# Optimization experiments

Measured on AMD Instinct MI355X. Metric: run time of the kernel, lower is better.

The kernel has to match this reference:

```python
import jax, jax.numpy as jnp
import numpy as np

N_NODES = 50000
N_EDGES = 800000
D_IN = 256
D_HID = 256
D_OUT = 256
BN_EPS = 1e-5
NORM_EPS = 1e-12


def _glorot(key, out_dim, in_dim):
    a = np.sqrt(6.0 / (in_dim + out_dim)).astype(np.float32)
    return jax.random.uniform(key, (out_dim, in_dim), jnp.float32, -a, a)


def setup_inputs() -> dict:
    key = jax.random.key(0)
    ks = jax.random.split(key, 8)
    x = jax.random.normal(ks[0], (N_NODES, D_IN), jnp.float32)
    edge_index = jax.random.randint(ks[1], (2, N_EDGES), 0, N_NODES, dtype=jnp.int32)
    batch = jnp.zeros((N_NODES,), jnp.int32)
    return {
        "x": x,
        "W1_l": _glorot(ks[2], D_HID, D_IN),
        "b1_l": jnp.zeros((D_HID,), jnp.float32),
        "W1_r": _glorot(ks[3], D_HID, D_IN),
        "W2_l": _glorot(ks[4], D_OUT, D_HID),
        "b2_l": jnp.zeros((D_OUT,), jnp.float32),
        "W2_r": _glorot(ks[5], D_OUT, D_HID),
        "gamma1": jnp.ones((D_HID,), jnp.float32),
        "beta1": jnp.zeros((D_HID,), jnp.float32),
        "edge_index": edge_index,
        "batch": batch,
    }


def _sage_conv(x, W_l, b_l, W_r, src, dst, n_nodes):
    # PyG SAGEConv (aggr='mean'): out = lin_l(mean_j x_j) + lin_r(x)
    msgs = x[src]                                            # [E, d] gather
    s = jax.ops.segment_sum(msgs, dst, num_segments=n_nodes)  # [N, d] scatter-add
    cnt = jax.ops.segment_sum(jnp.ones((src.shape[0], 1), x.dtype), dst,
                              num_segments=n_nodes)
    agg = jnp.where(cnt > 0, s / jnp.maximum(cnt, 1.0), 0.0)
    return agg @ W_l.T + b_l + x @ W_r.T


def _batch_norm(h, gamma, beta):
    mu = jnp.mean(h, axis=0)
    var = jnp.mean((h - mu) ** 2, axis=0)  # biased, as torch train-mode BN
    return (h - mu) * jax.lax.rsqrt(var + BN_EPS) * gamma + beta


def _l2_normalize(h):
    n = jnp.linalg.norm(h, axis=-1, keepdims=True)
    return h / jnp.maximum(n, NORM_EPS)


def reference(x, W1_l, b1_l, W1_r, W2_l, b2_l, W2_r, gamma1, beta1,
              edge_index, batch):
    n = x.shape[0]
    src, dst = edge_index[0], edge_index[1]
    # layer 1: SAGEConv -> BN (train stats) -> ReLU (dropout = identity in eval)
    h = _sage_conv(x, W1_l, b1_l, W1_r, src, dst, n)
    h = jax.nn.relu(_batch_norm(h, gamma1, beta1))
    # layer 2: SAGEConv -> L2 normalize
    h = _sage_conv(h, W2_l, b2_l, W2_r, src, dst, n)
    node_emb = _l2_normalize(h)
    # global mean pool over batch ids (single graph here), then normalize
    gsum = jax.ops.segment_sum(node_emb, batch, num_segments=1)
    gcnt = jax.ops.segment_sum(jnp.ones((n, 1), node_emb.dtype), batch,
                               num_segments=1)
    graph_emb = _l2_normalize(gsum / jnp.maximum(gcnt, 1.0))
    return node_emb, graph_emb
```

## Files before the change

kernel.cpp:

```cpp
#include <hip/hip_runtime.h>
#include <math.h>

#define NN 50000
#define NE 800000
#define D  256
#define SCB 196

typedef unsigned short u16;
typedef __attribute__((ext_vector_type(8))) short short8;
typedef __attribute__((ext_vector_type(8))) unsigned short u16x8;
typedef __attribute__((ext_vector_type(4))) float f32x4;

__device__ __forceinline__ u16 f2b(float f) {
    unsigned u = __float_as_uint(f);
    return (u16)((u + 0x7FFFu + ((u >> 16) & 1u)) >> 16);
}
__device__ __forceinline__ float b2f(u16 b) {
    return __uint_as_float(((unsigned)b) << 16);
}

__device__ __forceinline__ void gl16(const u16* g, u16* l) {
    __builtin_amdgcn_global_load_lds(
        (const __attribute__((address_space(1))) void*)g,
        (__attribute__((address_space(3))) void*)l, 16, 0, 0);
}

__global__ void degree_kernel(const int* __restrict__ dst, int* __restrict__ deg) {
    int e0 = (blockIdx.x * blockDim.x + threadIdx.x) * 4;
    if (e0 + 3 < NE) {
        int4 d = *(const int4*)&dst[e0];
        atomicAdd(&deg[d.x], 1);
        atomicAdd(&deg[d.y], 1);
        atomicAdd(&deg[d.z], 1);
        atomicAdd(&deg[d.w], 1);
    } else {
        for (int e = e0; e < NE; e++) atomicAdd(&deg[dst[e]], 1);
    }
}

__global__ void scanA_kernel(const int* __restrict__ deg, int* __restrict__ partial) {
    int t = threadIdx.x;
    int i = blockIdx.x * 256 + t;
    int v = (i < NN) ? deg[i] : 0;
#pragma unroll
    for (int o = 32; o; o >>= 1) v += __shfl_xor(v, o);
    __shared__ int sm[4];
    if ((t & 63) == 0) sm[t >> 6] = v;
    __syncthreads();
    if (t == 0) partial[blockIdx.x] = sm[0] + sm[1] + sm[2] + sm[3];
}

__global__ void scanB_kernel(const int* __restrict__ partial, int* __restrict__ base,
                             int* __restrict__ offs) {
    __shared__ int sm[256];
    int t = threadIdx.x;
    int v = (t < SCB) ? partial[t] : 0;
    sm[t] = v;
    __syncthreads();
    for (int off = 1; off < 256; off <<= 1) {
        int u = 0;
        if (t >= off) u = sm[t - off];
        __syncthreads();
        sm[t] += u;
        __syncthreads();
    }
    if (t < SCB) base[t] = sm[t] - v;
    if (t == 255) offs[NN] = sm[255];
}

__global__ void scanC_kernel(const int* __restrict__ deg, const int* __restrict__ base,
                             int* __restrict__ offs, int* __restrict__ cur) {
    __shared__ int sm[256];
    int t = threadIdx.x;
    int i = blockIdx.x * 256 + t;
    int v = (i < NN) ? deg[i] : 0;
    sm[t] = v;
    __syncthreads();
    for (int off = 1; off < 256; off <<= 1) {
        int u = 0;
        if (t >= off) u = sm[t - off];
        __syncthreads();
        sm[t] += u;
        __syncthreads();
    }
    int o = base[blockIdx.x] + sm[t] - v;
    if (i < NN) {
        offs[i] = o;
        cur[i] = o;
    }
}

__global__ void fill_kernel(const int* __restrict__ src, const int* __restrict__ dst,
                            int* __restrict__ cur, int* __restrict__ csr) {
    int e0 = (blockIdx.x * blockDim.x + threadIdx.x) * 4;
    if (e0 + 3 < NE) {
        int4 d = *(const int4*)&dst[e0];
        int4 s = *(const int4*)&src[e0];
        int p0 = atomicAdd(&cur[d.x], 1);
        int p1 = atomicAdd(&cur[d.y], 1);
        int p2 = atomicAdd(&cur[d.z], 1);
        int p3 = atomicAdd(&cur[d.w], 1);
        csr[p0] = s.x;
        csr[p1] = s.y;
        csr[p2] = s.z;
        csr[p3] = s.w;
    } else {
        for (int e = e0; e < NE; e++) {
            int pos = atomicAdd(&cur[dst[e]], 1);
            csr[pos] = src[e];
        }
    }
}

__global__ void wconv_kernel(const float* __restrict__ W1l, const float* __restrict__ W1r,
                             const float* __restrict__ W2l, const float* __restrict__ W2r,
                             u16* __restrict__ Wcat1, u16* __restrict__ Wcat2) {
    int r = blockIdx.x;
    int j = threadIdx.x;
    Wcat1[r * 512 + j]       = f2b(W1l[r * 256 + j]);
    Wcat1[r * 512 + 256 + j] = f2b(W1r[r * 256 + j]);
    Wcat2[r * 512 + j]       = f2b(W2l[r * 256 + j]);
    Wcat2[r * 512 + 256 + j] = f2b(W2r[r * 256 + j]);
}

__global__ void xconv_kernel(const float* __restrict__ x, u16* __restrict__ Acat) {
    int idx = blockIdx.x * blockDim.x + threadIdx.x;
    int r = idx >> 6;
    int c4 = (idx & 63) * 4;
    float4 v = *(const float4*)&x[(size_t)r * 256 + c4];
    ushort4 o;
    o.x = f2b(v.x); o.y = f2b(v.y); o.z = f2b(v.z); o.w = f2b(v.w);
    *(ushort4*)&Acat[(size_t)r * 512 + 256 + c4] = o;
}

__global__ __launch_bounds__(256)
void agg_kernel(const u16* __restrict__ Acat, const int* __restrict__ csr,
                const int* __restrict__ offs, u16* __restrict__ AcatW) {
    int wid = (blockIdx.x * blockDim.x + threadIdx.x) >> 6;
    int lane = threadIdx.x & 63;
    if (wid >= NN) return;
    int beg = offs[wid];
    int end = offs[wid + 1];
    int deg = end - beg;
    int half = lane >> 5;
    int lc = (lane & 31) * 8;
    int mid = beg + ((deg + 1) >> 1);
    int e  = half ? mid : beg;
    int hi = half ? end : mid;
    float a[8] = {0.f, 0.f, 0.f, 0.f, 0.f, 0.f, 0.f, 0.f};
    for (; e + 7 < hi; e += 8) {
        int s0 = csr[e + 0], s1 = csr[e + 1], s2 = csr[e + 2], s3 = csr[e + 3];
        int s4 = csr[e + 4], s5 = csr[e + 5], s6 = csr[e + 6], s7 = csr[e + 7];
        u16x8 v0 = *(const u16x8*)&Acat[(size_t)s0 * 512 + 256 + lc];
        u16x8 v1 = *(const u16x8*)&Acat[(size_t)s1 * 512 + 256 + lc];
        u16x8 v2 = *(const u16x8*)&Acat[(size_t)s2 * 512 + 256 + lc];
        u16x8 v3 = *(const u16x8*)&Acat[(size_t)s3 * 512 + 256 + lc];
        u16x8 v4 = *(const u16x8*)&Acat[(size_t)s4 * 512 + 256 + lc];
        u16x8 v5 = *(const u16x8*)&Acat[(size_t)s5 * 512 + 256 + lc];
        u16x8 v6 = *(const u16x8*)&Acat[(size_t)s6 * 512 + 256 + lc];
        u16x8 v7 = *(const u16x8*)&Acat[(size_t)s7 * 512 + 256 + lc];
#pragma unroll
        for (int i = 0; i < 8; i++)
            a[i] += ((b2f(v0[i]) + b2f(v1[i])) + (b2f(v2[i]) + b2f(v3[i]))) +
                    ((b2f(v4[i]) + b2f(v5[i])) + (b2f(v6[i]) + b2f(v7[i])));
    }
    for (; e + 3 < hi; e += 4) {
        int s0 = csr[e + 0], s1 = csr[e + 1], s2 = csr[e + 2], s3 = csr[e + 3];
        u16x8 v0 = *(const u16x8*)&Acat[(size_t)s0 * 512 + 256 + lc];
        u16x8 v1 = *(const u16x8*)&Acat[(size_t)s1 * 512 + 256 + lc];
        u16x8 v2 = *(const u16x8*)&Acat[(size_t)s2 * 512 + 256 + lc];
        u16x8 v3 = *(const u16x8*)&Acat[(size_t)s3 * 512 + 256 + lc];
#pragma unroll
        for (int i = 0; i < 8; i++)
            a[i] += (b2f(v0[i]) + b2f(v1[i])) + (b2f(v2[i]) + b2f(v3[i]));
    }
    for (; e < hi; e++) {
        int s0 = csr[e];
        u16x8 v0 = *(const u16x8*)&Acat[(size_t)s0 * 512 + 256 + lc];
#pragma unroll
        for (int i = 0; i < 8; i++) a[i] += b2f(v0[i]);
    }
#pragma unroll
    for (int i = 0; i < 8; i++) a[i] += __shfl_xor(a[i], 32);
    float sc = (deg > 0) ? 1.0f / (float)deg : 0.0f;
    if (half == 0) {
        u16x8 o;
#pragma unroll
        for (int i = 0; i < 8; i++) o[i] = f2b(a[i] * sc);
        *(u16x8*)&AcatW[(size_t)wid * 512 + lc] = o;
    }
}

template<int BF16_OUT>
__global__ __launch_bounds__(256)
void mfma_gemm_kernel(const u16* __restrict__ A, const u16* __restrict__ W,
                      const float* __restrict__ bias, void* __restrict__ Cout) {
    __shared__ u16 As[3][128 * 32];
    __shared__ u16 Bs[3][128 * 32];
    const int tid = threadIdx.x;
    const int l = tid & 63;
    const int wid = tid >> 6;
    const int wr = wid >> 1, wc = wid & 1;
    const int row0 = blockIdx.x * 128;
    const int col0 = blockIdx.y * 128;

    const u16* aptr[2];
    const u16* bptr[2];
#pragma unroll
    for (int i = 0; i < 2; i++) {
        int row = wid * 32 + i * 16 + (l >> 2);
        int kg = (l & 3) ^ ((row >> 1) & 3);
        int ra = row0 + row;
        if (ra > NN - 1) ra = NN - 1;
        aptr[i] = A + (size_t)ra * 512 + kg * 8;
        bptr[i] = W + (size_t)(col0 + row) * 512 + kg * 8;
    }

    f32x4 acc[4][4] = {};

#define STAGE(b, t)                                                          \
    do {                                                                     \
        _Pragma("unroll") for (int i_ = 0; i_ < 2; i_++) {                   \
            u16* al = &As[b][(wid * 32 + i_ * 16) * 32];                     \
            u16* bl = &Bs[b][(wid * 32 + i_ * 16) * 32];                     \
            gl16(aptr[i_] + (t) * 32, al);                                   \
            gl16(bptr[i_] + (t) * 32, bl);                                   \
        }                                                                    \
    } while (0)

    STAGE(0, 0);
    STAGE(1, 1);

    const int kq = l >> 4;
    const int sw = ((l & 15) >> 1) & 3;
#pragma unroll
    for (int t = 0; t < 16; t++) {
        if (t < 15) asm volatile("s_waitcnt vmcnt(4)" ::: "memory");
        else        asm volatile("s_waitcnt vmcnt(0)" ::: "memory");
        __builtin_amdgcn_s_barrier();
        __builtin_amdgcn_sched_barrier(0);

        if (t + 2 < 16) STAGE((t + 2) % 3, t + 2);

        short8 af[4], bf[4];
#pragma unroll
        for (int m = 0; m < 4; m++) {
            int row = wr * 64 + m * 16 + (l & 15);
            af[m] = *(const short8*)&As[t % 3][row * 32 + (kq ^ sw) * 8];
        }
#pragma unroll
        for (int n = 0; n < 4; n++) {
            int row = wc * 64 + n * 16 + (l & 15);
            bf[n] = *(const short8*)&Bs[t % 3][row * 32 + (kq ^ sw) * 8];
        }
#pragma unroll
        for (int m = 0; m < 4; m++)
#pragma unroll
            for (int n = 0; n < 4; n++)
                acc[m][n] = __builtin_amdgcn_mfma_f32_16x16x32_bf16(
                    af[m], bf[n], acc[m][n], 0, 0, 0);
    }
#undef STAGE

    const int cq = l >> 4;
    const int cc = l & 15;
#pragma unroll
    for (int m = 0; m < 4; m++) {
#pragma unroll
        for (int n = 0; n < 4; n++) {
            int c = col0 + wc * 64 + n * 16 + cc;
#pragma unroll
            for (int j = 0; j < 4; j++) {
                int r = row0 + wr * 64 + m * 16 + cq * 4 + j;
                if (r < NN) {
                    float v = acc[m][n][j] + bias[c];
                    if (BF16_OUT)
                        ((u16*)Cout)[(size_t)r * 256 + c] = f2b(v);
                    else
                        ((float*)Cout)[(size_t)r * 256 + c] = v;
                }
            }
        }
    }
}

__global__ void colstats_kernel(const u16* __restrict__ h, float* __restrict__ stats) {
    int j = threadIdx.x;
    float s0 = 0.f, s1 = 0.f;
    for (int r = blockIdx.x; r < NN; r += gridDim.x) {
        float v = b2f(h[(size_t)r * 256 + j]);
        s0 += v;
        s1 += v * v;
    }
    atomicAdd(&stats[j], s0);
    atomicAdd(&stats[256 + j], s1);
}

__global__ void bnfin_kernel(const float* __restrict__ stats,
                             const float* __restrict__ gamma,
                             const float* __restrict__ beta,
                             float* __restrict__ scale,
                             float* __restrict__ shift) {
    int j = threadIdx.x;
    const float invN = 1.0f / (float)NN;
    float mu = stats[j] * invN;
    float var = stats[256 + j] * invN - mu * mu;
    float sc = gamma[j] * rsqrtf(var + 1e-5f);
    scale[j] = sc;
    shift[j] = beta[j] - mu * sc;
}

__global__ void bnrelu_kernel(const u16* __restrict__ hb,
                              const float* __restrict__ scale,
                              const float* __restrict__ shift,
                              u16* __restrict__ Acat) {
    int idx = blockIdx.x * blockDim.x + threadIdx.x;
    int r = idx >> 5;
    int c8 = (idx & 31) * 8;
    u16x8 v = *(const u16x8*)&hb[(size_t)r * 256 + c8];
    u16x8 o;
#pragma unroll
    for (int i = 0; i < 8; i++) {
        float f = b2f(v[i]) * scale[c8 + i] + shift[c8 + i];
        o[i] = f2b(fmaxf(f, 0.f));
    }
    *(u16x8*)&Acat[(size_t)r * 512 + 256 + c8] = o;
}

__global__ __launch_bounds__(512)
void l2norm_kernel(float* __restrict__ out, float* __restrict__ gsum) {
    __shared__ float sm[8 * 256];
    int wave = threadIdx.x >> 6;
    int lane = threadIdx.x & 63;
    float c0 = 0.f, c1 = 0.f, c2 = 0.f, c3 = 0.f;
    for (int r = blockIdx.x * 8 + wave; r < NN; r += gridDim.x * 8) {
        float4 v = *(float4*)&out[(size_t)r * 256 + lane * 4];
        float sq = v.x * v.x + v.y * v.y + v.z * v.z + v.w * v.w;
#pragma unroll
        for (int o = 32; o; o >>= 1) sq += __shfl_xor(sq, o);
        float invn = 1.0f / fmaxf(sqrtf(sq), 1e-12f);
        v.x *= invn; v.y *= invn; v.z *= invn; v.w *= invn;
        *(float4*)&out[(size_t)r * 256 + lane * 4] = v;
        c0 += v.x; c1 += v.y; c2 += v.z; c3 += v.w;
    }
    *(float4*)&sm[wave * 256 + lane * 4] = make_float4(c0, c1, c2, c3);
    __syncthreads();
    int t = threadIdx.x;
    if (t < 256) {
        float s = 0.f;
#pragma unroll
        for (int w = 0; w < 8; w++) s += sm[w * 256 + t];
        atomicAdd(&gsum[t], s);
    }
}

__global__ void graph_kernel(const float* __restrict__ gsum, float* __restrict__ gout) {
    __shared__ float wsum[4];
    int j = threadIdx.x;
    float v = gsum[j] * (1.0f / (float)NN);
    float sq = v * v;
#pragma unroll
    for (int o = 32; o; o >>= 1) sq += __shfl_xor(sq, o);
    if ((j & 63) == 0) wsum[j >> 6] = sq;
    __syncthreads();
    float tot = wsum[0] + wsum[1] + wsum[2] + wsum[3];
    gout[j] = v / fmaxf(sqrtf(tot), 1e-12f);
}

extern "C" void kernel_launch(void* const* d_in, const int* in_sizes, int n_in,
                              void* d_out, int out_size, void* d_ws, size_t ws_size,
                              hipStream_t stream) {
    const float* x      = (const float*)d_in[0];
    const float* W1_l   = (const float*)d_in[1];
    const float* b1_l   = (const float*)d_in[2];
    const float* W1_r   = (const float*)d_in[3];
    const float* W2_l   = (const float*)d_in[4];
    const float* b2_l   = (const float*)d_in[5];
    const float* W2_r   = (const float*)d_in[6];
    const float* gamma1 = (const float*)d_in[7];
    const float* beta1  = (const float*)d_in[8];
    const int*   eidx   = (const int*)d_in[9];
    const int* src = eidx;
    const int* dst = eidx + NE;

    char* wsb = (char*)d_ws;
    int*   deg   = (int*)(wsb + 0);
    int*   offs  = (int*)(wsb + 200000);
    int*   cur   = (int*)(wsb + 400004);
    int*   csr   = (int*)(wsb + 600004);
    int*   part  = (int*)(wsb + 3800064);
    int*   base  = (int*)(wsb + 3801088);
    float* stats = (float*)(wsb + 3802112);
    float* gsum  = (float*)(wsb + 3804160);
    float* scale = (float*)(wsb + 3805184);
    float* shift = (float*)(wsb + 3806208);
    u16*   Wcat1 = (u16*)(wsb + 3807232);
    u16*   Wcat2 = (u16*)(wsb + 4069376);
    u16*   hb    = (u16*)(wsb + 4331520);
    u16*   Acat  = (u16*)(wsb + 29931520);
    float* out   = (float*)d_out;
    float* gout  = out + (size_t)NN * 256;

    hipMemsetAsync(deg, 0, NN * sizeof(int), stream);
    hipMemsetAsync(stats, 0, 3072, stream);

    wconv_kernel<<<256, 256, 0, stream>>>(W1_l, W1_r, W2_l, W2_r, Wcat1, Wcat2);
    xconv_kernel<<<12500, 256, 0, stream>>>(x, Acat);

    degree_kernel<<<(NE / 4 + 255) / 256, 256, 0, stream>>>(dst, deg);
    scanA_kernel<<<SCB, 256, 0, stream>>>(deg, part);
    scanB_kernel<<<1, 256, 0, stream>>>(part, base, offs);
    scanC_kernel<<<SCB, 256, 0, stream>>>(deg, base, offs, cur);
    fill_kernel<<<(NE / 4 + 255) / 256, 256, 0, stream>>>(src, dst, cur, csr);

    dim3 ggrid((NN + 127) / 128, 2);

    agg_kernel<<<12500, 256, 0, stream>>>(Acat, csr, offs, Acat);
    mfma_gemm_kernel<1><<<ggrid, 256, 0, stream>>>(Acat, Wcat1, b1_l, hb);
    colstats_kernel<<<512, 256, 0, stream>>>(hb, stats);
    bnfin_kernel<<<1, 256, 0, stream>>>(stats, gamma1, beta1, scale, shift);
    bnrelu_kernel<<<6250, 256, 0, stream>>>(hb, scale, shift, Acat);

    agg_kernel<<<12500, 256, 0, stream>>>(Acat, csr, offs, Acat);
    mfma_gemm_kernel<0><<<ggrid, 256, 0, stream>>>(Acat, Wcat2, b2_l, out);

    l2norm_kernel<<<1024, 512, 0, stream>>>(out, gsum);
    graph_kernel<<<1, 256, 0, stream>>>(gsum, gout);
}
```

Before: 408.7 us.

## Merge conversion kernels, fold BN finalize into BN-ReLU, use per-wave GEMM staging

The weight and input bf16 conversion kernels become a single launch, and the BN finalize kernel is folded into the BN+ReLU kernel, where each block recomputes scale and shift into shared memory. The GEMM now gives each wave its own double-buffered LDS region holding only its own 64-row A and B slices, so the block-wide barrier per k-step goes away. In exchange each wave loads twice as much data (A and B are duplicated across waves), LDS use per block grows, and every BN block redoes the 256-column finalize.

```diff
diff --git a/kernel.cpp b/kernel.cpp
--- a/kernel.cpp
+++ b/kernel.cpp
@@ -112,25 +112,28 @@
     }
 }
 
-__global__ void wconv_kernel(const float* __restrict__ W1l, const float* __restrict__ W1r,
-                             const float* __restrict__ W2l, const float* __restrict__ W2r,
-                             u16* __restrict__ Wcat1, u16* __restrict__ Wcat2) {
-    int r = blockIdx.x;
-    int j = threadIdx.x;
-    Wcat1[r * 512 + j]       = f2b(W1l[r * 256 + j]);
-    Wcat1[r * 512 + 256 + j] = f2b(W1r[r * 256 + j]);
-    Wcat2[r * 512 + j]       = f2b(W2l[r * 256 + j]);
-    Wcat2[r * 512 + 256 + j] = f2b(W2r[r * 256 + j]);
-}
-
-__global__ void xconv_kernel(const float* __restrict__ x, u16* __restrict__ Acat) {
-    int idx = blockIdx.x * blockDim.x + threadIdx.x;
-    int r = idx >> 6;
-    int c4 = (idx & 63) * 4;
-    float4 v = *(const float4*)&x[(size_t)r * 256 + c4];
-    ushort4 o;
-    o.x = f2b(v.x); o.y = f2b(v.y); o.z = f2b(v.z); o.w = f2b(v.w);
-    *(ushort4*)&Acat[(size_t)r * 512 + 256 + c4] = o;
+__global__ void wxconv_kernel(const float* __restrict__ x,
+                              const float* __restrict__ W1l, const float* __restrict__ W1r,
+                              const float* __restrict__ W2l, const float* __restrict__ W2r,
+                              u16* __restrict__ Acat,
+                              u16* __restrict__ Wcat1, u16* __restrict__ Wcat2) {
+    int b = blockIdx.x;
+    if (b < 12500) {
+        int idx = b * 256 + threadIdx.x;
+        int r = idx >> 6;
+        int c4 = (idx & 63) * 4;
+        float4 v = *(const float4*)&x[(size_t)r * 256 + c4];
+        ushort4 o;
+        o.x = f2b(v.x); o.y = f2b(v.y); o.z = f2b(v.z); o.w = f2b(v.w);
+        *(ushort4*)&Acat[(size_t)r * 512 + 256 + c4] = o;
+    } else {
+        int r = b - 12500;
+        int j = threadIdx.x;
+        Wcat1[r * 512 + j]       = f2b(W1l[r * 256 + j]);
+        Wcat1[r * 512 + 256 + j] = f2b(W1r[r * 256 + j]);
+        Wcat2[r * 512 + j]       = f2b(W2l[r * 256 + j]);
+        Wcat2[r * 512 + 256 + j] = f2b(W2r[r * 256 + j]);
+    }
 }
 
 __global__ __launch_bounds__(256)
@@ -195,8 +198,7 @@
 __global__ __launch_bounds__(256)
 void mfma_gemm_kernel(const u16* __restrict__ A, const u16* __restrict__ W,
                       const float* __restrict__ bias, void* __restrict__ Cout) {
-    __shared__ u16 As[3][128 * 32];
-    __shared__ u16 Bs[3][128 * 32];
+    __shared__ u16 S[4][2][2][64 * 32];
     const int tid = threadIdx.x;
     const int l = tid & 63;
     const int wid = tid >> 6;
@@ -204,55 +206,52 @@
     const int row0 = blockIdx.x * 128;
     const int col0 = blockIdx.y * 128;
 
-    const u16* aptr[2];
-    const u16* bptr[2];
-#pragma unroll
-    for (int i = 0; i < 2; i++) {
-        int row = wid * 32 + i * 16 + (l >> 2);
-        int kg = (l & 3) ^ ((row >> 1) & 3);
-        int ra = row0 + row;
+    const u16* aptr[4];
+    const u16* bptr[4];
+#pragma unroll
+    for (int i = 0; i < 4; i++) {
+        int rl = i * 16 + (l >> 2);
+        int kg = (l & 3) ^ ((rl >> 1) & 3);
+        int ra = row0 + wr * 64 + rl;
         if (ra > NN - 1) ra = NN - 1;
         aptr[i] = A + (size_t)ra * 512 + kg * 8;
-        bptr[i] = W + (size_t)(col0 + row) * 512 + kg * 8;
+        bptr[i] = W + (size_t)(col0 + wc * 64 + rl) * 512 + kg * 8;
     }
 
     f32x4 acc[4][4] = {};
 
-#define STAGE(b, t)                                                          \
-    do {                                                                     \
-        _Pragma("unroll") for (int i_ = 0; i_ < 2; i_++) {                   \
-            u16* al = &As[b][(wid * 32 + i_ * 16) * 32];                     \
-            u16* bl = &Bs[b][(wid * 32 + i_ * 16) * 32];                     \
-            gl16(aptr[i_] + (t) * 32, al);                                   \
-            gl16(bptr[i_] + (t) * 32, bl);                                   \
-        }                                                                    \
+#define STAGE(b, t)                                                     \
+    do {                                                                \
+        _Pragma("unroll") for (int i_ = 0; i_ < 4; i_++) {              \
+            gl16(aptr[i_] + (t) * 32, &S[wid][b][0][i_ * 16 * 32]);     \
+            gl16(bptr[i_] + (t) * 32, &S[wid][b][1][i_ * 16 * 32]);     \
+        }                                                               \
     } while (0)
 
     STAGE(0, 0);
-    STAGE(1, 1);
 
     const int kq = l >> 4;
     const int sw = ((l & 15) >> 1) & 3;
+    const int slot = (kq ^ sw) * 8;
 #pragma unroll
     for (int t = 0; t < 16; t++) {
-        if (t < 15) asm volatile("s_waitcnt vmcnt(4)" ::: "memory");
-        else        asm volatile("s_waitcnt vmcnt(0)" ::: "memory");
-        __builtin_amdgcn_s_barrier();
+        if (t < 15) {
+            STAGE((t + 1) & 1, t + 1);
+            asm volatile("s_waitcnt vmcnt(8)" ::: "memory");
+        } else {
+            asm volatile("s_waitcnt vmcnt(0)" ::: "memory");
+        }
         __builtin_amdgcn_sched_barrier(0);
 
-        if (t + 2 < 16) STAGE((t + 2) % 3, t + 2);
-
+        const u16* As = &S[wid][t & 1][0][0];
+        const u16* Bs = &S[wid][t & 1][1][0];
         short8 af[4], bf[4];
 #pragma unroll
-        for (int m = 0; m < 4; m++) {
-            int row = wr * 64 + m * 16 + (l & 15);
-            af[m] = *(const short8*)&As[t % 3][row * 32 + (kq ^ sw) * 8];
-        }
-#pragma unroll
-        for (int n = 0; n < 4; n++) {
-            int row = wc * 64 + n * 16 + (l & 15);
-            bf[n] = *(const short8*)&Bs[t % 3][row * 32 + (kq ^ sw) * 8];
-        }
+        for (int m = 0; m < 4; m++)
+            af[m] = *(const short8*)&As[(m * 16 + (l & 15)) * 32 + slot];
+#pragma unroll
+        for (int n = 0; n < 4; n++)
+            bf[n] = *(const short8*)&Bs[(n * 16 + (l & 15)) * 32 + slot];
 #pragma unroll
         for (int m = 0; m < 4; m++)
 #pragma unroll
@@ -296,32 +295,30 @@
     atomicAdd(&stats[256 + j], s1);
 }
 
-__global__ void bnfin_kernel(const float* __restrict__ stats,
-                             const float* __restrict__ gamma,
-                             const float* __restrict__ beta,
-                             float* __restrict__ scale,
-                             float* __restrict__ shift) {
-    int j = threadIdx.x;
-    const float invN = 1.0f / (float)NN;
-    float mu = stats[j] * invN;
-    float var = stats[256 + j] * invN - mu * mu;
-    float sc = gamma[j] * rsqrtf(var + 1e-5f);
-    scale[j] = sc;
-    shift[j] = beta[j] - mu * sc;
-}
-
 __global__ void bnrelu_kernel(const u16* __restrict__ hb,
-                              const float* __restrict__ scale,
-                              const float* __restrict__ shift,
+                              const float* __restrict__ stats,
+                              const float* __restrict__ gamma,
+                              const float* __restrict__ beta,
                               u16* __restrict__ Acat) {
-    int idx = blockIdx.x * blockDim.x + threadIdx.x;
+    __shared__ float s_scale[256], s_shift[256];
+    int t = threadIdx.x;
+    {
+        const float invN = 1.0f / (float)NN;
+        float mu = stats[t] * invN;
+        float var = stats[256 + t] * invN - mu * mu;
+        float sc = gamma[t] * rsqrtf(var + 1e-5f);
+        s_scale[t] = sc;
+        s_shift[t] = beta[t] - mu * sc;
+    }
+    __syncthreads();
+    int idx = blockIdx.x * 256 + t;
     int r = idx >> 5;
     int c8 = (idx & 31) * 8;
     u16x8 v = *(const u16x8*)&hb[(size_t)r * 256 + c8];
     u16x8 o;
 #pragma unroll
     for (int i = 0; i < 8; i++) {
-        float f = b2f(v[i]) * scale[c8 + i] + shift[c8 + i];
+        float f = b2f(v[i]) * s_scale[c8 + i] + s_shift[c8 + i];
         o[i] = f2b(fmaxf(f, 0.f));
     }
     *(u16x8*)&Acat[(size_t)r * 512 + 256 + c8] = o;
@@ -392,8 +389,6 @@
     int*   base  = (int*)(wsb + 3801088);
     float* stats = (float*)(wsb + 3802112);
     float* gsum  = (float*)(wsb + 3804160);
-    float* scale = (float*)(wsb + 3805184);
-    float* shift = (float*)(wsb + 3806208);
     u16*   Wcat1 = (u16*)(wsb + 3807232);
     u16*   Wcat2 = (u16*)(wsb + 4069376);
     u16*   hb    = (u16*)(wsb + 4331520);
@@ -404,8 +399,8 @@
     hipMemsetAsync(deg, 0, NN * sizeof(int), stream);
     hipMemsetAsync(stats, 0, 3072, stream);
 
-    wconv_kernel<<<256, 256, 0, stream>>>(W1_l, W1_r, W2_l, W2_r, Wcat1, Wcat2);
-    xconv_kernel<<<12500, 256, 0, stream>>>(x, Acat);
+    wxconv_kernel<<<12756, 256, 0, stream>>>(x, W1_l, W1_r, W2_l, W2_r,
+                                             Acat, Wcat1, Wcat2);
 
     degree_kernel<<<(NE / 4 + 255) / 256, 256, 0, stream>>>(dst, deg);
     scanA_kernel<<<SCB, 256, 0, stream>>>(deg, part);
@@ -418,8 +413,7 @@
     agg_kernel<<<12500, 256, 0, stream>>>(Acat, csr, offs, Acat);
     mfma_gemm_kernel<1><<<ggrid, 256, 0, stream>>>(Acat, Wcat1, b1_l, hb);
     colstats_kernel<<<512, 256, 0, stream>>>(hb, stats);
-    bnfin_kernel<<<1, 256, 0, stream>>>(stats, gamma1, beta1, scale, shift);
-    bnrelu_kernel<<<6250, 256, 0, stream>>>(hb, scale, shift, Acat);
+    bnrelu_kernel<<<6250, 256, 0, stream>>>(hb, stats, gamma1, beta1, Acat);
 
     agg_kernel<<<12500, 256, 0, stream>>>(Acat, csr, offs, Acat);
     mfma_gemm_kernel<0><<<ggrid, 256, 0, stream>>>(Acat, Wcat2, b2_l, out);
```

Result: no change. 400.7 us (-1.9%).
